# Kernel tuning notes

Measured on AMD Instinct MI355X. Metric: run time of the kernel, lower is better.

## Reference

```python
import jax, jax.numpy as jnp
import numpy as np

N = 50000   # nodes
E = 600000  # edges
D = 128     # input_dim
H = 128     # hidden_dim
C = 1       # num_classes
EPS = 1e-5


def _glorot(key, fan_in, fan_out):
    s = (2.0 / (fan_in + fan_out)) ** 0.5
    return jax.random.normal(key, (fan_in, fan_out), jnp.float32) * s


def setup_inputs() -> dict:
    key = jax.random.key(0)
    ks = jax.random.split(key, 16)
    inp = {
        "x": jax.random.normal(ks[0], (N, D), jnp.float32),
        "edge_index": jax.random.randint(ks[1], (2, E), 0, N, dtype=jnp.int64),
        # GCN layer 0: D -> H, layers 1,2: H -> H
        "W0": _glorot(ks[2], D, H), "b0": jnp.zeros((H,), jnp.float32),
        "g0": jnp.ones((H,), jnp.float32), "be0": jnp.zeros((H,), jnp.float32),
        "W1": _glorot(ks[3], H, H), "b1": jnp.zeros((H,), jnp.float32),
        "g1": jnp.ones((H,), jnp.float32), "be1": jnp.zeros((H,), jnp.float32),
        "W2": _glorot(ks[4], H, H), "b2": jnp.zeros((H,), jnp.float32),
        "g2": jnp.ones((H,), jnp.float32), "be2": jnp.zeros((H,), jnp.float32),
        # MLP head: Linear(H,H) -> ReLU -> Linear(H,C)
        "hW1": _glorot(ks[5], H, H), "hb1": jnp.zeros((H,), jnp.float32),
        "hW2": _glorot(ks[6], H, C), "hb2": jnp.zeros((C,), jnp.float32),
    }
    return inp


def _layer_norm(h, g, b):
    mu = jnp.mean(h, axis=-1, keepdims=True)
    var = jnp.mean(jnp.square(h - mu), axis=-1, keepdims=True)
    return (h - mu) * jax.lax.rsqrt(var + EPS) * g + b


def reference(x, edge_index, W0, b0, g0, be0, W1, b1, g1, be1, W2, b2, g2, be2,
              hW1, hb1, hW2, hb2):
    # --- GCN normalization (add self-loops, symmetric deg^-1/2 norm) ---
    loop = jnp.arange(N, dtype=edge_index.dtype)
    src = jnp.concatenate([edge_index[0], loop])  # [E+N]
    dst = jnp.concatenate([edge_index[1], loop])  # [E+N]
    deg = jax.ops.segment_sum(jnp.ones_like(dst, jnp.float32), dst, num_segments=N)
    dinv = jax.lax.rsqrt(deg)  # deg >= 1 due to self-loops
    norm = (dinv[src] * dinv[dst])[:, None]  # [E+N, 1]

    def gcn_layer(h, W, b, g, be):
        hW = h @ W                                   # [N, H] dense GEMM
        msg = hW[src] * norm                         # gather + scale  [E+N, H]
        agg = jax.ops.segment_sum(msg, dst, num_segments=N) + b
        return jax.nn.relu(_layer_norm(agg, g, be))  # dropout = identity (eval)

    h = gcn_layer(x, W0, b0, g0, be0)
    h = gcn_layer(h, W1, b1, g1, be1)
    h = gcn_layer(h, W2, b2, g2, be2)

    # MLP head
    h = jax.nn.relu(h @ hW1 + hb1)
    logits = h @ hW2 + hb2  # [N, C]
    return logits
```

## Files before the change

kernel.cpp:

```cpp
#include <hip/hip_runtime.h>
#include <hip/hip_fp16.h>

#define N_NODES 50000
#define N_EDGES 600000
#define HDIM 128
#define EPS 1e-5f

typedef __attribute__((ext_vector_type(8))) short bf16x8;
typedef __attribute__((ext_vector_type(4))) float f32x4;
typedef __attribute__((ext_vector_type(4))) _Float16 h16x4;
typedef __attribute__((ext_vector_type(8))) _Float16 h16x8;

__global__ void detect_kernel(const int* __restrict__ ei, int* __restrict__ flag) {
    __shared__ int nonzero;
    if (threadIdx.x == 0) nonzero = 0;
    __syncthreads();
    int acc = 0;
    for (int i = threadIdx.x; i < 1024; i += blockDim.x)
        acc |= ei[2 * i + 1];
    if (acc) atomicOr(&nonzero, 1);
    __syncthreads();
    if (threadIdx.x == 0) *flag = (nonzero == 0) ? 1 : 0;
}

__device__ __forceinline__ int load_idx(const int* __restrict__ ei, int pos, int f) {
    return f ? ei[2 * pos] : ei[pos];
}

__global__ void cvt_x(const float* __restrict__ x, _Float16* __restrict__ xh) {
    int idx = blockIdx.x * 256 + threadIdx.x;
    if (idx >= N_NODES * 32) return;
    float4 v = ((const float4*)x)[idx];
    h16x4 o;
    o[0] = (_Float16)v.x; o[1] = (_Float16)v.y; o[2] = (_Float16)v.z; o[3] = (_Float16)v.w;
    ((h16x4*)xh)[idx] = o;
}

__global__ void deg_kernel(const int* __restrict__ ei, const int* __restrict__ flag,
                           int* __restrict__ deg, int* __restrict__ slot) {
    int e = blockIdx.x * blockDim.x + threadIdx.x;
    if (e >= N_EDGES) return;
    int f = *flag;
    int d = load_idx(ei, N_EDGES + e, f);
    slot[e] = atomicAdd(&deg[d], 1);
}

__global__ void block_sum(const int* __restrict__ deg, int* __restrict__ bsum,
                          float* __restrict__ dinv) {
    __shared__ int sm[256];
    int i = blockIdx.x * 256 + threadIdx.x;
    int d = (i < N_NODES) ? deg[i] : 0;
    if (i < N_NODES) dinv[i] = rsqrtf((float)d + 1.0f);
    sm[threadIdx.x] = d;
    __syncthreads();
    for (int s = 128; s > 0; s >>= 1) {
        if (threadIdx.x < s) sm[threadIdx.x] += sm[threadIdx.x + s];
        __syncthreads();
    }
    if (threadIdx.x == 0) bsum[blockIdx.x] = sm[0];
}

__global__ void scan_bsums(const int* __restrict__ bsum, int* __restrict__ boff, int nb) {
    __shared__ int sm[256];
    int t = threadIdx.x;
    int v = (t < nb) ? bsum[t] : 0;
    sm[t] = v;
    __syncthreads();
    for (int s = 1; s < 256; s <<= 1) {
        int add = (t >= s) ? sm[t - s] : 0;
        __syncthreads();
        sm[t] += add;
        __syncthreads();
    }
    if (t < nb) boff[t] = sm[t] - v;
}

__global__ void scan_block(const int* __restrict__ deg, const int* __restrict__ boff,
                           int* __restrict__ rowst) {
    __shared__ int sm[256];
    int t = threadIdx.x;
    int i = blockIdx.x * 256 + t;
    int v = (i < N_NODES) ? deg[i] : 0;
    sm[t] = v;
    __syncthreads();
    for (int s = 1; s < 256; s <<= 1) {
        int add = (t >= s) ? sm[t - s] : 0;
        __syncthreads();
        sm[t] += add;
        __syncthreads();
    }
    int excl = boff[blockIdx.x] + sm[t] - v;
    if (i < N_NODES) rowst[i] = excl;
    if (i == N_NODES - 1) rowst[N_NODES] = excl + v;
}

__global__ void scatter_kernel(const int* __restrict__ ei, const int* __restrict__ flag,
                               const int* __restrict__ rowst, const float* __restrict__ dinv,
                               const int* __restrict__ slot, unsigned* __restrict__ ecsr) {
    int e = blockIdx.x * blockDim.x + threadIdx.x;
    if (e >= N_EDGES) return;
    if (e < 16) ecsr[N_EDGES + e] = 0u;
    int f = *flag;
    int s = load_idx(ei, e, f);
    int d = load_idx(ei, N_EDGES + e, f);
    int pos = rowst[d] + slot[e];
    _Float16 wv = (_Float16)dinv[s];
    unsigned wb = (unsigned)__builtin_bit_cast(unsigned short, wv);
    ecsr[pos] = (wb << 16) | (unsigned)s;
}

__device__ __forceinline__ float unpack_w(unsigned p) {
    unsigned short b = (unsigned short)(p >> 16);
    return (float)__builtin_bit_cast(_Float16, b);
}

__global__ __launch_bounds__(256) void agg_kernel(const _Float16* __restrict__ h,
                                                  const float* __restrict__ dinv,
                                                  const int* __restrict__ rowst,
                                                  const unsigned* __restrict__ ecsr,
                                                  _Float16* __restrict__ out) {
    int node = blockIdx.x * 16 + (threadIdx.x >> 4);
    int sub = threadIdx.x & 15;
    if (node >= N_NODES) return;
    const h16x8* h8 = (const h16x8*)h;
    float dd = dinv[node];
    h16x8 v = h8[(size_t)node * 16 + sub];
    float acc[8];
#pragma unroll
    for (int i = 0; i < 8; ++i) acc[i] = dd * (float)v[i];
    int e1 = rowst[node + 1];
    for (int e = rowst[node]; e < e1; e += 4) {
        unsigned p0 = ecsr[e];
        unsigned p1 = ecsr[e + 1];
        unsigned p2 = ecsr[e + 2];
        unsigned p3 = ecsr[e + 3];
        int s0 = p0 & 0xFFFFu;
        float w0 = unpack_w(p0);
        int s1 = (e + 1 < e1) ? (int)(p1 & 0xFFFFu) : s0;
        float w1 = (e + 1 < e1) ? unpack_w(p1) : 0.f;
        int s2 = (e + 2 < e1) ? (int)(p2 & 0xFFFFu) : s0;
        float w2 = (e + 2 < e1) ? unpack_w(p2) : 0.f;
        int s3 = (e + 3 < e1) ? (int)(p3 & 0xFFFFu) : s0;
        float w3 = (e + 3 < e1) ? unpack_w(p3) : 0.f;
        h16x8 u0 = h8[(size_t)s0 * 16 + sub];
        h16x8 u1 = h8[(size_t)s1 * 16 + sub];
        h16x8 u2 = h8[(size_t)s2 * 16 + sub];
        h16x8 u3 = h8[(size_t)s3 * 16 + sub];
#pragma unroll
        for (int i = 0; i < 8; ++i) {
            acc[i] += w0 * (float)u0[i];
            acc[i] += w1 * (float)u1[i];
            acc[i] += w2 * (float)u2[i];
            acc[i] += w3 * (float)u3[i];
        }
    }
    h16x8 r;
#pragma unroll
    for (int i = 0; i < 8; ++i) r[i] = (_Float16)(acc[i] * dd);
    ((h16x8*)out)[(size_t)node * 16 + sub] = r;
}

__device__ __forceinline__ void bsplit(float a, short& hi, short& lo) {
    unsigned u = __float_as_uint(a);
    unsigned r = (u + 0x7FFFu + ((u >> 16) & 1u)) & 0xFFFF0000u;
    hi = (short)(r >> 16);
    float l = a - __uint_as_float(r);
    unsigned ul = __float_as_uint(l);
    unsigned rl = ul + 0x7FFFu + ((ul >> 16) & 1u);
    lo = (short)(rl >> 16);
}

__global__ void pack_w(const float* __restrict__ W0, const float* __restrict__ W1,
                       const float* __restrict__ W2, const float* __restrict__ W3,
                       short* __restrict__ pkh, short* __restrict__ pkl) {
    const float* W = (blockIdx.y == 0) ? W0 : (blockIdx.y == 1) ? W1
                   : (blockIdx.y == 2) ? W2 : W3;
    int idx = blockIdx.x * 256 + threadIdx.x;
    int lane = idx & 63;
    int cf = (idx >> 6) & 7;
    int ks = idx >> 9;
    int col = cf * 16 + (lane & 15);
    int k0 = ks * 32 + (lane >> 4) * 8;
    short h[8], l[8];
#pragma unroll
    for (int i = 0; i < 8; ++i) bsplit(W[(size_t)(k0 + i) * HDIM + col], h[i], l[i]);
    size_t base = (size_t)blockIdx.y * 16384 + (size_t)idx * 8;
#pragma unroll
    for (int i = 0; i < 8; ++i) { pkh[base + i] = h[i]; pkl[base + i] = l[i]; }
}

__global__ __launch_bounds__(256) void gemm_mfma(const _Float16* __restrict__ A,
                                                 const short* __restrict__ Bh,
                                                 const short* __restrict__ Bl,
                                                 const float* __restrict__ bias,
                                                 const float* __restrict__ gamma,
                                                 const float* __restrict__ beta,
                                                 void* __restrict__ outraw,
                                                 int mode, int nrows) {
    int t = threadIdx.x;
    int wave = t >> 6, lane = t & 63;
    int lrow = lane & 15, lk = lane >> 4;
    int rowb = blockIdx.x * 64 + wave * 16;

    f32x4 acc[8];
#pragma unroll
    for (int cf = 0; cf < 8; ++cf) acc[cf] = (f32x4){0.f, 0.f, 0.f, 0.f};

    const _Float16* arow = A + (size_t)(rowb + lrow) * HDIM;

#pragma unroll
    for (int ks = 0; ks < 4; ++ks) {
        h16x8 a = *(const h16x8*)(arow + ks * 32 + lk * 8);
        bf16x8 ah, al;
#pragma unroll
        for (int i = 0; i < 8; ++i) {
            short hh, ll;
            bsplit((float)a[i], hh, ll);
            ah[i] = hh; al[i] = ll;
        }
        const short* bhp = Bh + (size_t)(ks * 8) * 512 + (size_t)lane * 8;
        const short* blp = Bl + (size_t)(ks * 8) * 512 + (size_t)lane * 8;
#pragma unroll
        for (int cf = 0; cf < 8; ++cf) {
            bf16x8 bh = *(const bf16x8*)(bhp + (size_t)cf * 512);
            bf16x8 bl = *(const bf16x8*)(blp + (size_t)cf * 512);
            acc[cf] = __builtin_amdgcn_mfma_f32_16x16x32_bf16(ah, bh, acc[cf], 0, 0, 0);
            acc[cf] = __builtin_amdgcn_mfma_f32_16x16x32_bf16(ah, bl, acc[cf], 0, 0, 0);
            acc[cf] = __builtin_amdgcn_mfma_f32_16x16x32_bf16(al, bh, acc[cf], 0, 0, 0);
            acc[cf] = __builtin_amdgcn_mfma_f32_16x16x32_bf16(al, bl, acc[cf], 0, 0, 0);
        }
    }

    float bias_v[8];
#pragma unroll
    for (int cf = 0; cf < 8; ++cf) bias_v[cf] = bias[cf * 16 + lrow];

    if (mode == 0) {
        _Float16* out = (_Float16*)outraw;
        float gam[8], bet[8];
#pragma unroll
        for (int cf = 0; cf < 8; ++cf) {
            gam[cf] = gamma[cf * 16 + lrow];
            bet[cf] = beta[cf * 16 + lrow];
        }
#pragma unroll
        for (int r = 0; r < 4; ++r) {
            float vv[8];
            float s1 = 0.f;
#pragma unroll
            for (int cf = 0; cf < 8; ++cf) {
                vv[cf] = acc[cf][r] + bias_v[cf];
                s1 += vv[cf];
            }
#pragma unroll
            for (int m = 1; m <= 8; m <<= 1) s1 += __shfl_xor(s1, m);
            float mean = s1 * (1.0f / 128.0f);
            float s2 = 0.f;
            float cc[8];
#pragma unroll
            for (int cf = 0; cf < 8; ++cf) {
                cc[cf] = vv[cf] - mean;
                s2 += cc[cf] * cc[cf];
            }
#pragma unroll
            for (int m = 1; m <= 8; m <<= 1) s2 += __shfl_xor(s2, m);
            float var = s2 * (1.0f / 128.0f);
            float rs = rsqrtf(var + EPS);
            int row = rowb + lk * 4 + r;
            if (row < nrows) {
#pragma unroll
                for (int cf = 0; cf < 8; ++cf) {
                    float y = cc[cf] * rs * gam[cf] + bet[cf];
                    out[(size_t)row * HDIM + cf * 16 + lrow] = (_Float16)(y > 0.f ? y : 0.f);
                }
            }
        }
    } else {
        float* out = (float*)outraw;
        float w2v[8];
#pragma unroll
        for (int cf = 0; cf < 8; ++cf) w2v[cf] = gamma[cf * 16 + lrow];
        float b2 = beta[0];
#pragma unroll
        for (int r = 0; r < 4; ++r) {
            float part = 0.f;
#pragma unroll
            for (int cf = 0; cf < 8; ++cf) {
                float y = acc[cf][r] + bias_v[cf];
                y = y > 0.f ? y : 0.f;
                part += y * w2v[cf];
            }
#pragma unroll
            for (int m = 1; m <= 8; m <<= 1) part += __shfl_xor(part, m);
            int row = rowb + lk * 4 + r;
            if (row < nrows && lrow == 0) out[row] = part + b2;
        }
    }
}

extern "C" void kernel_launch(void* const* d_in, const int* in_sizes, int n_in,
                              void* d_out, int out_size, void* d_ws, size_t ws_size,
                              hipStream_t stream) {
    (void)in_sizes; (void)n_in; (void)out_size; (void)ws_size;
    const float* x   = (const float*)d_in[0];
    const int*   ei  = (const int*)d_in[1];
    const float* W0  = (const float*)d_in[2];
    const float* b0  = (const float*)d_in[3];
    const float* g0  = (const float*)d_in[4];
    const float* be0 = (const float*)d_in[5];
    const float* W1  = (const float*)d_in[6];
    const float* b1  = (const float*)d_in[7];
    const float* g1  = (const float*)d_in[8];
    const float* be1 = (const float*)d_in[9];
    const float* W2  = (const float*)d_in[10];
    const float* b2  = (const float*)d_in[11];
    const float* g2  = (const float*)d_in[12];
    const float* be2 = (const float*)d_in[13];
    const float* hW1 = (const float*)d_in[14];
    const float* hb1 = (const float*)d_in[15];
    const float* hW2 = (const float*)d_in[16];
    const float* hb2 = (const float*)d_in[17];
    float* out = (float*)d_out;

    char* w = (char*)d_ws;
    size_t off = 0;
    auto alloc = [&](size_t bytes) -> void* {
        void* p = w + off;
        off += (bytes + 255) & ~(size_t)255;
        return p;
    };
    float*     dinv  = (float*)alloc((size_t)N_NODES * 4);
    int*       deg   = (int*)alloc((size_t)N_NODES * 4);
    int*       rowst = (int*)alloc((size_t)(N_NODES + 1) * 4);
    int*       slot  = (int*)alloc((size_t)N_EDGES * 4);
    unsigned*  ecsr  = (unsigned*)alloc((size_t)(N_EDGES + 16) * 4);
    int*       bsum  = (int*)alloc(256 * 4);
    int*       boff  = (int*)alloc(256 * 4);
    int*       flag  = (int*)alloc(256);
    _Float16*  hagg  = (_Float16*)alloc((size_t)N_NODES * HDIM * 2);
    _Float16*  xh    = (_Float16*)alloc((size_t)N_NODES * HDIM * 2);
    _Float16*  hA    = (_Float16*)alloc((size_t)N_NODES * HDIM * 2);
    _Float16*  hB    = (_Float16*)alloc((size_t)N_NODES * HDIM * 2);
    short*     pkh   = (short*)alloc((size_t)4 * 16384 * 2);
    short*     pkl   = (short*)alloc((size_t)4 * 16384 * 2);

    hipMemsetAsync(deg, 0, (size_t)N_NODES * 4, stream);

    detect_kernel<<<1, 256, 0, stream>>>(ei, flag);
    cvt_x<<<(N_NODES * 32 + 255) / 256, 256, 0, stream>>>(x, xh);
    deg_kernel<<<(N_EDGES + 255) / 256, 256, 0, stream>>>(ei, flag, deg, slot);
    int nb = (N_NODES + 255) / 256;
    block_sum<<<nb, 256, 0, stream>>>(deg, bsum, dinv);
    scan_bsums<<<1, 256, 0, stream>>>(bsum, boff, nb);
    scan_block<<<nb, 256, 0, stream>>>(deg, boff, rowst);
    scatter_kernel<<<(N_EDGES + 255) / 256, 256, 0, stream>>>(ei, flag, rowst, dinv, slot, ecsr);

    dim3 pg(8, 4);
    pack_w<<<pg, 256, 0, stream>>>(W0, W1, W2, hW1, pkh, pkl);

    int nab = (N_NODES + 15) / 16;
    int ngb = (N_NODES + 63) / 64;
    agg_kernel<<<nab, 256, 0, stream>>>(xh, dinv, rowst, ecsr, hagg);
    gemm_mfma<<<ngb, 256, 0, stream>>>(hagg, pkh, pkl, b0, g0, be0, hA, 0, N_NODES);
    agg_kernel<<<nab, 256, 0, stream>>>(hA, dinv, rowst, ecsr, hagg);
    gemm_mfma<<<ngb, 256, 0, stream>>>(hagg, pkh + (size_t)16384, pkl + (size_t)16384,
                                       b1, g1, be1, hB, 0, N_NODES);
    agg_kernel<<<nab, 256, 0, stream>>>(hB, dinv, rowst, ecsr, hagg);
    gemm_mfma<<<ngb, 256, 0, stream>>>(hagg, pkh + (size_t)2 * 16384, pkl + (size_t)2 * 16384,
                                       b2, g2, be2, hA, 0, N_NODES);
    gemm_mfma<<<ngb, 256, 0, stream>>>(hA, pkh + (size_t)3 * 16384, pkl + (size_t)3 * 16384,
                                       hb1, hW2, hb2, out, 1, N_NODES);
}
```

Baseline: 201.7 us.

## Use fp16 MFMA with split weights and merge prep kernels into one launch

The GEMM no longer splits activations into bf16 hi/lo parts. Since activations are already fp16, it runs two fp16 MFMAs per fragment (A times W_hi and A times W_lo) instead of four bf16 MFMAs, and the per-element split arithmetic is removed. The x conversion, degree counting and weight packing kernels are fused into one launch distinguished by block ranges, which removes launch overhead. Precision now relies on fp16 range for weights and the split residual.

```diff
diff --git a/kernel.cpp b/kernel.cpp
--- a/kernel.cpp
+++ b/kernel.cpp
@@ -6,10 +6,13 @@
 #define HDIM 128
 #define EPS 1e-5f
 
-typedef __attribute__((ext_vector_type(8))) short bf16x8;
 typedef __attribute__((ext_vector_type(4))) float f32x4;
 typedef __attribute__((ext_vector_type(4))) _Float16 h16x4;
 typedef __attribute__((ext_vector_type(8))) _Float16 h16x8;
+
+#define CVT_BLKS 6250
+#define DEG_BLKS ((N_EDGES + 255) / 256)
+#define PACK_BLKS 32
 
 __global__ void detect_kernel(const int* __restrict__ ei, int* __restrict__ flag) {
     __shared__ int nonzero;
@@ -27,22 +30,52 @@
     return f ? ei[2 * pos] : ei[pos];
 }
 
-__global__ void cvt_x(const float* __restrict__ x, _Float16* __restrict__ xh) {
-    int idx = blockIdx.x * 256 + threadIdx.x;
-    if (idx >= N_NODES * 32) return;
-    float4 v = ((const float4*)x)[idx];
-    h16x4 o;
-    o[0] = (_Float16)v.x; o[1] = (_Float16)v.y; o[2] = (_Float16)v.z; o[3] = (_Float16)v.w;
-    ((h16x4*)xh)[idx] = o;
-}
-
-__global__ void deg_kernel(const int* __restrict__ ei, const int* __restrict__ flag,
-                           int* __restrict__ deg, int* __restrict__ slot) {
-    int e = blockIdx.x * blockDim.x + threadIdx.x;
-    if (e >= N_EDGES) return;
-    int f = *flag;
-    int d = load_idx(ei, N_EDGES + e, f);
-    slot[e] = atomicAdd(&deg[d], 1);
+__device__ __forceinline__ void hsplit(float a, _Float16& hi, _Float16& lo) {
+    _Float16 h = (_Float16)a;
+    hi = h;
+    lo = (_Float16)(a - (float)h);
+}
+
+__global__ void prep_kernel(const float* __restrict__ x, _Float16* __restrict__ xh,
+                            const int* __restrict__ ei, const int* __restrict__ flag,
+                            int* __restrict__ deg, int* __restrict__ slot,
+                            const float* __restrict__ W0, const float* __restrict__ W1,
+                            const float* __restrict__ W2, const float* __restrict__ W3,
+                            _Float16* __restrict__ pkh, _Float16* __restrict__ pkl) {
+    int b = blockIdx.x;
+    if (b < CVT_BLKS) {
+        int idx = b * 256 + threadIdx.x;
+        if (idx < N_NODES * 32) {
+            float4 v = ((const float4*)x)[idx];
+            h16x4 o;
+            o[0] = (_Float16)v.x; o[1] = (_Float16)v.y;
+            o[2] = (_Float16)v.z; o[3] = (_Float16)v.w;
+            ((h16x4*)xh)[idx] = o;
+        }
+    } else if (b < CVT_BLKS + DEG_BLKS) {
+        int e = (b - CVT_BLKS) * 256 + threadIdx.x;
+        if (e < N_EDGES) {
+            int f = *flag;
+            int d = load_idx(ei, N_EDGES + e, f);
+            slot[e] = atomicAdd(&deg[d], 1);
+        }
+    } else {
+        int pb = b - CVT_BLKS - DEG_BLKS;
+        int wsel = pb >> 3;
+        const float* W = (wsel == 0) ? W0 : (wsel == 1) ? W1 : (wsel == 2) ? W2 : W3;
+        int idx = (pb & 7) * 256 + threadIdx.x;
+        int lane = idx & 63;
+        int cf = (idx >> 6) & 7;
+        int ks = idx >> 9;
+        int col = cf * 16 + (lane & 15);
+        int k0 = ks * 32 + (lane >> 4) * 8;
+        _Float16 h[8], l[8];
+#pragma unroll
+        for (int i = 0; i < 8; ++i) hsplit(W[(size_t)(k0 + i) * HDIM + col], h[i], l[i]);
+        size_t base = (size_t)wsel * 16384 + (size_t)idx * 8;
+#pragma unroll
+        for (int i = 0; i < 8; ++i) { pkh[base + i] = h[i]; pkl[base + i] = l[i]; }
+    }
 }
 
 __global__ void block_sum(const int* __restrict__ deg, int* __restrict__ bsum,
@@ -160,38 +193,9 @@
     ((h16x8*)out)[(size_t)node * 16 + sub] = r;
 }
 
-__device__ __forceinline__ void bsplit(float a, short& hi, short& lo) {
-    unsigned u = __float_as_uint(a);
-    unsigned r = (u + 0x7FFFu + ((u >> 16) & 1u)) & 0xFFFF0000u;
-    hi = (short)(r >> 16);
-    float l = a - __uint_as_float(r);
-    unsigned ul = __float_as_uint(l);
-    unsigned rl = ul + 0x7FFFu + ((ul >> 16) & 1u);
-    lo = (short)(rl >> 16);
-}
-
-__global__ void pack_w(const float* __restrict__ W0, const float* __restrict__ W1,
-                       const float* __restrict__ W2, const float* __restrict__ W3,
-                       short* __restrict__ pkh, short* __restrict__ pkl) {
-    const float* W = (blockIdx.y == 0) ? W0 : (blockIdx.y == 1) ? W1
-                   : (blockIdx.y == 2) ? W2 : W3;
-    int idx = blockIdx.x * 256 + threadIdx.x;
-    int lane = idx & 63;
-    int cf = (idx >> 6) & 7;
-    int ks = idx >> 9;
-    int col = cf * 16 + (lane & 15);
-    int k0 = ks * 32 + (lane >> 4) * 8;
-    short h[8], l[8];
-#pragma unroll
-    for (int i = 0; i < 8; ++i) bsplit(W[(size_t)(k0 + i) * HDIM + col], h[i], l[i]);
-    size_t base = (size_t)blockIdx.y * 16384 + (size_t)idx * 8;
-#pragma unroll
-    for (int i = 0; i < 8; ++i) { pkh[base + i] = h[i]; pkl[base + i] = l[i]; }
-}
-
 __global__ __launch_bounds__(256) void gemm_mfma(const _Float16* __restrict__ A,
-                                                 const short* __restrict__ Bh,
-                                                 const short* __restrict__ Bl,
+                                                 const _Float16* __restrict__ Bh,
+                                                 const _Float16* __restrict__ Bl,
                                                  const float* __restrict__ bias,
                                                  const float* __restrict__ gamma,
                                                  const float* __restrict__ beta,
@@ -211,23 +215,14 @@
 #pragma unroll
     for (int ks = 0; ks < 4; ++ks) {
         h16x8 a = *(const h16x8*)(arow + ks * 32 + lk * 8);
-        bf16x8 ah, al;
-#pragma unroll
-        for (int i = 0; i < 8; ++i) {
-            short hh, ll;
-            bsplit((float)a[i], hh, ll);
-            ah[i] = hh; al[i] = ll;
-        }
-        const short* bhp = Bh + (size_t)(ks * 8) * 512 + (size_t)lane * 8;
-        const short* blp = Bl + (size_t)(ks * 8) * 512 + (size_t)lane * 8;
+        const _Float16* bhp = Bh + (size_t)(ks * 8) * 512 + (size_t)lane * 8;
+        const _Float16* blp = Bl + (size_t)(ks * 8) * 512 + (size_t)lane * 8;
 #pragma unroll
         for (int cf = 0; cf < 8; ++cf) {
-            bf16x8 bh = *(const bf16x8*)(bhp + (size_t)cf * 512);
-            bf16x8 bl = *(const bf16x8*)(blp + (size_t)cf * 512);
-            acc[cf] = __builtin_amdgcn_mfma_f32_16x16x32_bf16(ah, bh, acc[cf], 0, 0, 0);
-            acc[cf] = __builtin_amdgcn_mfma_f32_16x16x32_bf16(ah, bl, acc[cf], 0, 0, 0);
-            acc[cf] = __builtin_amdgcn_mfma_f32_16x16x32_bf16(al, bh, acc[cf], 0, 0, 0);
-            acc[cf] = __builtin_amdgcn_mfma_f32_16x16x32_bf16(al, bl, acc[cf], 0, 0, 0);
+            h16x8 bh = *(const h16x8*)(bhp + (size_t)cf * 512);
+            h16x8 bl = *(const h16x8*)(blp + (size_t)cf * 512);
+            acc[cf] = __builtin_amdgcn_mfma_f32_16x16x32_f16(a, bh, acc[cf], 0, 0, 0);
+            acc[cf] = __builtin_amdgcn_mfma_f32_16x16x32_f16(a, bl, acc[cf], 0, 0, 0);
         }
     }
 
@@ -341,22 +336,19 @@
     _Float16*  xh    = (_Float16*)alloc((size_t)N_NODES * HDIM * 2);
     _Float16*  hA    = (_Float16*)alloc((size_t)N_NODES * HDIM * 2);
     _Float16*  hB    = (_Float16*)alloc((size_t)N_NODES * HDIM * 2);
-    short*     pkh   = (short*)alloc((size_t)4 * 16384 * 2);
-    short*     pkl   = (short*)alloc((size_t)4 * 16384 * 2);
+    _Float16*  pkh   = (_Float16*)alloc((size_t)4 * 16384 * 2);
+    _Float16*  pkl   = (_Float16*)alloc((size_t)4 * 16384 * 2);
 
     hipMemsetAsync(deg, 0, (size_t)N_NODES * 4, stream);
 
     detect_kernel<<<1, 256, 0, stream>>>(ei, flag);
-    cvt_x<<<(N_NODES * 32 + 255) / 256, 256, 0, stream>>>(x, xh);
-    deg_kernel<<<(N_EDGES + 255) / 256, 256, 0, stream>>>(ei, flag, deg, slot);
+    prep_kernel<<<CVT_BLKS + DEG_BLKS + PACK_BLKS, 256, 0, stream>>>(
+        x, xh, ei, flag, deg, slot, W0, W1, W2, hW1, pkh, pkl);
     int nb = (N_NODES + 255) / 256;
     block_sum<<<nb, 256, 0, stream>>>(deg, bsum, dinv);
     scan_bsums<<<1, 256, 0, stream>>>(bsum, boff, nb);
     scan_block<<<nb, 256, 0, stream>>>(deg, boff, rowst);
     scatter_kernel<<<(N_EDGES + 255) / 256, 256, 0, stream>>>(ei, flag, rowst, dinv, slot, ecsr);
-
-    dim3 pg(8, 4);
-    pack_w<<<pg, 256, 0, stream>>>(W0, W1, W2, hW1, pkh, pkl);
 
     int nab = (N_NODES + 15) / 16;
     int ngb = (N_NODES + 63) / 64;
```

Measured after the change: 190.5 us. 1.06x faster.
